# Kernel tuning notes

Measured on AMD Instinct MI355X. Metric: run time of the kernel, lower is better.

The kernel has to match this reference:

```python
import jax, jax.numpy as jnp
import numpy as np
from jax import lax

N, D, K = 8192, 512, 16
EPS = 1e-8


def _safe_sqrt(x):
    # sqrt with a guard so vjp is finite at exact zeros (diagonal of dist matrix)
    return jnp.where(x > 0, jnp.sqrt(jnp.maximum(x, 1e-12)), 0.0)


def _pairwise_dist(a):
    # [n, d] -> [n, n] euclidean distances via Gram trick
    sq = jnp.sum(a * a, axis=-1)
    d2 = sq[:, None] + sq[None, :] - 2.0 * (a @ a.T)
    return _safe_sqrt(d2)


def _curvature_proxy(emb, k):
    n = emb.shape[0]
    dists = _pairwise_dist(emb)  # [n, n]
    neg_d, knn_idx = lax.top_k(-dists, k + 1)  # k+1 smallest
    knn_dists = -neg_d[:, 1:]   # drop self [n, k]
    knn_idx = knn_idx[:, 1:]    # [n, k]
    avg_dist_to_neighbors = knn_dists.mean(axis=1)  # [n]

    nb = emb[knn_idx]  # [n, k, d] gathered neighbor embeddings
    nsq = jnp.sum(nb * nb, axis=-1)  # [n, k]
    gram = jnp.einsum('nkd,nld->nkl', nb, nb)  # [n, k, k]
    inter = _safe_sqrt(nsq[:, :, None] + nsq[:, None, :] - 2.0 * gram)

    mask = jnp.triu(jnp.ones((k, k), dtype=bool), 1)
    n_pairs = k * (k - 1) // 2
    inter_mean = jnp.sum(jnp.where(mask, inter, 0.0), axis=(1, 2)) / n_pairs  # [n]

    curvature = inter_mean / (avg_dist_to_neighbors + EPS)
    return curvature, knn_dists


def setup_inputs() -> dict:
    key = jax.random.key(0)
    k1, k2, k3 = jax.random.split(key, 3)
    embeddings = jax.random.normal(k1, (N, D), dtype=jnp.float32)
    ref_curvature = jax.random.uniform(k2, (N,), dtype=jnp.float32)
    ref_distances = jax.random.uniform(k3, (N, K), dtype=jnp.float32)
    return {"embeddings": embeddings, "ref_curvature": ref_curvature,
            "ref_distances": ref_distances}


def reference(embeddings, ref_curvature, ref_distances):
    curr_curv, curr_dists = _curvature_proxy(embeddings, K)
    curvature_loss = jnp.mean((curr_curv - ref_curvature) ** 2)
    scale_loss = (curr_dists.mean() - ref_distances.mean()) ** 2
    return curvature_loss + 0.1 * scale_loss
```

## Files before the change

kernel.cpp:

```cpp
#include <hip/hip_runtime.h>
#include <cfloat>
#include <cmath>
#include <stdint.h>

#define N 8192
#define D 512
#define K 16
#define RB 64
#define JS 2048
#define NSL (N / JS)
#define JT 128
#define NT (JS / JT)
#define KC 64
#define NCH (D / KC)
#define CAP 32
#define PB 64

typedef __bf16 bf16x8 __attribute__((ext_vector_type(8)));
typedef __bf16 bf16x4 __attribute__((ext_vector_type(4)));
typedef float  f32x16 __attribute__((ext_vector_type(16)));
typedef float  f32x4  __attribute__((ext_vector_type(4)));

__global__ __launch_bounds__(256)
void k_cast_sqnorm(const float* __restrict__ emb, float* __restrict__ sq,
                   __bf16* __restrict__ embh, int* __restrict__ kadjG) {
    int row = blockIdx.x * 4 + (threadIdx.x >> 6);
    int lane = threadIdx.x & 63;
    const float4* e = (const float4*)(emb + (size_t)row * D);
    float s = 0.f;
    #pragma unroll
    for (int c = 0; c < 2; c++) {
        float4 v = e[lane + 64 * c];
        s += v.x * v.x + v.y * v.y + v.z * v.z + v.w * v.w;
        bf16x4 h = { (__bf16)v.x, (__bf16)v.y, (__bf16)v.z, (__bf16)v.w };
        *(bf16x4*)&embh[(size_t)row * D + (size_t)(lane + 64 * c) * 4] = h;
    }
    for (int off = 32; off; off >>= 1) s += __shfl_down(s, off, 64);
    if (lane == 0) sq[row] = s;
    if (lane == 1) kadjG[row] = 0x7f7fffff;
}

__global__ __launch_bounds__(512)
void k_knn(const __bf16* __restrict__ embh, const float* __restrict__ sq,
           float* __restrict__ pd2, int* __restrict__ pidx,
           int* __restrict__ kadjG) {
    __shared__ __align__(16) __bf16 As[2][RB][KC + 8];
    __shared__ __align__(16) __bf16 Bs[2][JT][KC + 8];
    __shared__ float svD[RB][CAP + 1];
    __shared__ int   svI[RB][CAP + 1];
    __shared__ float sqr[RB];
    __shared__ float kadj[RB];
    __shared__ int   scount[RB];
    __shared__ int   again2[2];

    const int t   = threadIdx.x;
    const int rg  = blockIdx.x >> 2;
    const int sl  = blockIdx.x & 3;
    const int ib  = rg * RB;
    const int jsb = sl * JS;
    const int lane = t & 63, quad = lane >> 5, l31 = lane & 31;
    const int w  = t >> 6;
    const int wr = (w & 1) * 32;
    const int wc = (w >> 1) * 32;

    const int mrow = t >> 3, tid8 = t & 7;
    float l0 = FLT_MAX, l1 = FLT_MAX;
    int   i0 = 0, i1 = 0;
    float kmx = FLT_MAX;
    int   nfill = 0;

    if (t < RB) {
        sqr[t] = sq[ib + t];
        kadj[t] = FLT_MAX; scount[t] = 0;
    }
    __syncthreads();

    for (int jt = 0; jt < NT; jt++) {
        const int jb = jsb + jt * JT;
        f32x16 acc = {};

        {
            int row = t >> 3, g = t & 7;
            *(uint4*)&As[0][row][g * 8] = *(const uint4*)&embh[(size_t)(ib + row) * D + g * 8];
            #pragma unroll
            for (int q = 0; q < 2; q++) {
                int s = t + 512 * q;
                int brow = s >> 3, bg = s & 7;
                *(uint4*)&Bs[0][brow][bg * 8] = *(const uint4*)&embh[(size_t)(jb + brow) * D + bg * 8];
            }
        }
        __syncthreads();

        uint4 pfA, pfB[2];
        for (int kc = 0; kc < NCH; kc++) {
            const int cur = kc & 1;
            if (kc + 1 < NCH) {
                int k0 = (kc + 1) * KC;
                {
                    int row = t >> 3, g = t & 7;
                    pfA = *(const uint4*)&embh[(size_t)(ib + row) * D + k0 + g * 8];
                }
                #pragma unroll
                for (int q = 0; q < 2; q++) {
                    int s = t + 512 * q; int brow = s >> 3, bg = s & 7;
                    pfB[q] = *(const uint4*)&embh[(size_t)(jb + brow) * D + k0 + bg * 8];
                }
            }
            __builtin_amdgcn_s_setprio(1);
            #pragma unroll
            for (int kk = 0; kk < KC / 16; kk++) {
                int ko = kk * 16 + quad * 8;
                bf16x8 a0 = *(const bf16x8*)&As[cur][wr + l31][ko];
                bf16x8 b0 = *(const bf16x8*)&Bs[cur][wc + l31][ko];
                acc = __builtin_amdgcn_mfma_f32_32x32x16_bf16(a0, b0, acc, 0, 0, 0);
            }
            __builtin_amdgcn_s_setprio(0);
            if (kc + 1 < NCH) {
                {
                    int row = t >> 3, g = t & 7;
                    *(uint4*)&As[cur ^ 1][row][g * 8] = pfA;
                }
                #pragma unroll
                for (int q = 0; q < 2; q++) {
                    int s = t + 512 * q; int brow = s >> 3, bg = s & 7;
                    *(uint4*)&Bs[cur ^ 1][brow][bg * 8] = pfB[q];
                }
            }
            __syncthreads();
        }

        if (t < RB) {
            float g = __int_as_float(kadjG[ib + t]);
            kadj[t] = fminf(kadj[t], g - sqr[t]);
        }
        if (t == 0) again2[0] = 0;
        __syncthreads();

        float sqc0 = sq[jb + wc + l31];
        uint32_t mask = 0;
        int pass = 0;
        while (true) {
            #pragma unroll
            for (int reg = 0; reg < 16; reg++) {
                if ((mask >> reg) & 1) continue;
                int row_l = wr + ((reg & 3) + ((reg >> 2) << 3) + (quad << 2));
                float t2 = sqc0 - 2.f * acc[reg];
                if (t2 < kadj[row_l]) {
                    int j = jb + wc + l31;
                    if (j != ib + row_l) {
                        int p = atomicAdd(&scount[row_l], 1);
                        if (p < CAP) {
                            svD[row_l][p] = t2 + sqr[row_l];
                            svI[row_l][p] = j;
                            mask |= (1u << reg);
                        }
                    }
                }
            }
            __syncthreads();
            {
                int cnt = scount[mrow];
                if (cnt) {
                    int m = cnt < CAP ? cnt : CAP;
                    for (int p = 0; p < m; p++) {
                        float d2 = svD[mrow][p];
                        if (d2 < kmx) {
                            if (nfill < K) {
                                if ((nfill >> 1) == tid8) {
                                    int jv = svI[mrow][p];
                                    if ((nfill & 1) == 0) { l0 = d2; i0 = jv; }
                                    else                  { l1 = d2; i1 = jv; }
                                }
                                nfill++;
                                if (nfill == K) {
                                    float lm = fmaxf(l0, l1);
                                    #pragma unroll
                                    for (int off = 1; off < 8; off <<= 1)
                                        lm = fmaxf(lm, __shfl_xor(lm, off, 64));
                                    kmx = lm;
                                }
                            } else {
                                float mx = l0; int am = 0;
                                if (l1 > mx) { mx = l1; am = 1; }
                                int gam = (tid8 << 1) | am;
                                #pragma unroll
                                for (int off = 1; off < 8; off <<= 1) {
                                    float omx = __shfl_xor(mx, off, 64);
                                    int   oga = __shfl_xor(gam, off, 64);
                                    if (omx > mx || (omx == mx && oga < gam)) { mx = omx; gam = oga; }
                                }
                                if ((gam >> 1) == tid8) {
                                    int jv = svI[mrow][p];
                                    if ((gam & 1) == 0) { l0 = d2; i0 = jv; }
                                    else                { l1 = d2; i1 = jv; }
                                }
                                float lm = fmaxf(l0, l1);
                                #pragma unroll
                                for (int off = 1; off < 8; off <<= 1)
                                    lm = fmaxf(lm, __shfl_xor(lm, off, 64));
                                kmx = lm;
                            }
                        }
                    }
                    if (tid8 == 0) {
                        kadj[mrow] = fminf(kadj[mrow], kmx - sqr[mrow]);
                        scount[mrow] = 0;
                        if (cnt > CAP) again2[pass & 1] = 1;
                    }
                }
            }
            if (t == 0) again2[(pass + 1) & 1] = 0;
            __syncthreads();
            if (!again2[pass & 1]) break;
            pass++;
        }

        if (tid8 == 0 && kmx < FLT_MAX)
            atomicMin(&kadjG[ib + mrow], __float_as_int(kmx));
    }

    {
        size_t base = (size_t)(ib + mrow) * (NSL * K) + sl * K + tid8 * 2;
        pd2[base + 0] = l0; pd2[base + 1] = l1;
        pidx[base + 0] = i0; pidx[base + 1] = i1;
    }
}

__global__ __launch_bounds__(256)
void k_merge(const float* __restrict__ pd2, const int* __restrict__ pidx,
             int* __restrict__ knn, float* __restrict__ row_sum) {
    int row = blockIdx.x * 256 + threadIdx.x;
    float bd[K]; int bi[K];
    #pragma unroll
    for (int q = 0; q < K; q++) { bd[q] = FLT_MAX; bi[q] = 0; }
    float kmx = FLT_MAX;
    const float* pr = pd2 + (size_t)row * (NSL * K);
    const int*   pi = pidx + (size_t)row * (NSL * K);
    for (int s = 0; s < NSL * K; s++) {
        float d2 = pr[s];
        if (d2 < kmx) {
            int am = 0; float mx = bd[0];
            #pragma unroll
            for (int q = 1; q < K; q++) if (bd[q] > mx) { mx = bd[q]; am = q; }
            bd[am] = d2; bi[am] = pi[s];
            mx = bd[0];
            #pragma unroll
            for (int q = 1; q < K; q++) mx = fmaxf(mx, bd[q]);
            kmx = mx;
        }
    }
    float s = 0.f;
    #pragma unroll
    for (int q = 0; q < K; q++) {
        float d2 = bd[q];
        s += (d2 > 0.f) ? sqrtf(fmaxf(d2, 1e-12f)) : 0.f;
        knn[(size_t)row * K + q] = bi[q];
    }
    row_sum[row] = s;
}

__global__ __launch_bounds__(256)
void k_curv(const __bf16* __restrict__ embh, const int* __restrict__ knn_idx,
            const float* __restrict__ row_sum, const float* __restrict__ ref_curv,
            float* __restrict__ curv_err) {
    __shared__ __align__(16) __bf16 nb[4][K][D + 8];
    __shared__ float diagS[4][16];
    const int t = threadIdx.x;
    const int w = t >> 6, lane = t & 63;
    const int i = blockIdx.x * 4 + w;

    #pragma unroll
    for (int r = 0; r < K; r++) {
        int nidx = knn_idx[(size_t)i * K + r];
        *(uint4*)&nb[w][r][lane * 8] =
            *(const uint4*)&embh[(size_t)nidx * D + lane * 8];
    }
    __syncthreads();

    f32x4 acc = {};
    #pragma unroll
    for (int kc = 0; kc < D / 32; kc++) {
        bf16x8 a = *(const bf16x8*)&nb[w][lane & 15][(lane >> 4) * 8 + kc * 32];
        acc = __builtin_amdgcn_mfma_f32_16x16x32_bf16(a, a, acc, 0, 0, 0);
    }

    #pragma unroll
    for (int q = 0; q < 4; q++) {
        int r = (lane >> 4) * 4 + q;
        if (r == (lane & 15)) diagS[w][r] = acc[q];
    }
    __syncthreads();

    float s = 0.f;
    #pragma unroll
    for (int q = 0; q < 4; q++) {
        int r = (lane >> 4) * 4 + q, c = lane & 15;
        if (r != c) {
            float d2 = diagS[w][r] + diagS[w][c] - 2.f * acc[q];
            s += (d2 > 0.f) ? sqrtf(fmaxf(d2, 1e-12f)) : 0.f;
        }
    }
    #pragma unroll
    for (int off = 32; off; off >>= 1) s += __shfl_down(s, off, 64);

    if (lane == 0) {
        float inter_mean = (0.5f * s) / 120.f;
        float avg = row_sum[i] / 16.f;
        float curv = inter_mean / (avg + 1e-8f);
        float diff = curv - ref_curv[i];
        curv_err[i] = diff * diff;
    }
}

__global__ __launch_bounds__(256)
void k_part(const float* __restrict__ curv_err, const float* __restrict__ row_sum,
            const float* __restrict__ ref_dist, float* __restrict__ part) {
    const int b = blockIdx.x, t = threadIdx.x;
    const int gid = b * 256 + t;
    const int stride = PB * 256;
    float s1 = 0.f, s2 = 0.f, s3 = 0.f;
    for (int i = gid; i < N; i += stride) { s1 += curv_err[i]; s2 += row_sum[i]; }
    for (int i = gid; i < N * K; i += stride) s3 += ref_dist[i];
    for (int off = 32; off; off >>= 1) {
        s1 += __shfl_down(s1, off, 64);
        s2 += __shfl_down(s2, off, 64);
        s3 += __shfl_down(s3, off, 64);
    }
    __shared__ float a1[4], a2[4], a3[4];
    int w = t >> 6, lane = t & 63;
    if (lane == 0) { a1[w] = s1; a2[w] = s2; a3[w] = s3; }
    __syncthreads();
    if (t == 0) {
        float t1 = 0.f, t2 = 0.f, t3 = 0.f;
        #pragma unroll
        for (int q = 0; q < 4; q++) { t1 += a1[q]; t2 += a2[q]; t3 += a3[q]; }
        part[b] = t1; part[PB + b] = t2; part[2 * PB + b] = t3;
    }
}

__global__ __launch_bounds__(64)
void k_final2(const float* __restrict__ part, float* __restrict__ out) {
    const int t = threadIdx.x;
    float s1 = part[t], s2 = part[PB + t], s3 = part[2 * PB + t];
    for (int off = 32; off; off >>= 1) {
        s1 += __shfl_down(s1, off, 64);
        s2 += __shfl_down(s2, off, 64);
        s3 += __shfl_down(s3, off, 64);
    }
    if (t == 0) {
        float curv_loss = s1 / (float)N;
        float dm = s2 / (float)(N * K);
        float rm = s3 / (float)(N * K);
        float d = dm - rm;
        out[0] = curv_loss + 0.1f * d * d;
    }
}

extern "C" void kernel_launch(void* const* d_in, const int* in_sizes, int n_in,
                              void* d_out, int out_size, void* d_ws, size_t ws_size,
                              hipStream_t stream) {
    const float* emb      = (const float*)d_in[0];
    const float* ref_curv = (const float*)d_in[1];
    const float* ref_dist = (const float*)d_in[2];
    float* out = (float*)d_out;

    float*  sq       = (float*)d_ws;
    float*  row_sum  = sq + N;
    float*  curv_err = row_sum + N;
    float*  pd2      = curv_err + N;
    int*    pidx     = (int*)(pd2 + (size_t)N * NSL * K);
    int*    knn      = pidx + (size_t)N * NSL * K;
    __bf16* embh     = (__bf16*)(knn + (size_t)N * K);
    float*  part     = (float*)(embh + (size_t)N * D);
    int*    kadjG    = (int*)(part + 3 * PB);

    k_cast_sqnorm<<<N / 4, 256, 0, stream>>>(emb, sq, embh, kadjG);
    k_knn<<<(N / RB) * NSL, 512, 0, stream>>>(embh, sq, pd2, pidx, kadjG);
    k_merge<<<N / 256, 256, 0, stream>>>(pd2, pidx, knn, row_sum);
    k_curv<<<N / 4, 256, 0, stream>>>(embh, knn, row_sum, ref_curv, curv_err);
    k_part<<<PB, 256, 0, stream>>>(curv_err, row_sum, ref_dist, part);
    k_final2<<<1, 64, 0, stream>>>(part, out);
}
```

Measured before the change: 362.8 us.

## Flatten tile and K-chunk loops into one continuous double-buffered pipeline

Merges the per-column-tile loop and the K-chunk loop into one flattened loop unrolled by two, so the next tile's first chunks are prefetched while the current tile finishes. This removes the pipeline drain and refill at every tile boundary. Barriers now use a custom macro that waits only on LDS counters (lgkmcnt) instead of a full __syncthreads, and the kadjG global read is issued early into a register. The cost is more live prefetch registers and more complex control flow, and the hand-written barrier could miss a needed wait.

```diff
diff --git a/kernel.cpp b/kernel.cpp
--- a/kernel.cpp
+++ b/kernel.cpp
@@ -13,6 +13,7 @@
 #define NT (JS / JT)
 #define KC 64
 #define NCH (D / KC)
+#define TOT (NT * NCH)
 #define CAP 32
 #define PB 64
 
@@ -20,6 +21,12 @@
 typedef __bf16 bf16x4 __attribute__((ext_vector_type(4)));
 typedef float  f32x16 __attribute__((ext_vector_type(16)));
 typedef float  f32x4  __attribute__((ext_vector_type(4)));
+
+#define SYNCK() do {                                          \
+    asm volatile("s_waitcnt lgkmcnt(0)" ::: "memory");        \
+    __builtin_amdgcn_s_barrier();                             \
+    asm volatile("" ::: "memory");                            \
+} while (0)
 
 __global__ __launch_bounds__(256)
 void k_cast_sqnorm(const float* __restrict__ emb, float* __restrict__ sq,
@@ -63,160 +70,194 @@
     const int wr = (w & 1) * 32;
     const int wc = (w >> 1) * 32;
 
+    const int arow = t >> 3, ag = t & 7;
+
     const int mrow = t >> 3, tid8 = t & 7;
     float l0 = FLT_MAX, l1 = FLT_MAX;
     int   i0 = 0, i1 = 0;
     float kmx = FLT_MAX;
     int   nfill = 0;
+    float kg = FLT_MAX;
 
     if (t < RB) {
         sqr[t] = sq[ib + t];
         kadj[t] = FLT_MAX; scount[t] = 0;
     }
-    __syncthreads();
-
-    for (int jt = 0; jt < NT; jt++) {
-        const int jb = jsb + jt * JT;
-        f32x16 acc = {};
-
+
+    f32x16 acc = {};
+    uint4 pfA_e, pfB_e[2];
+    uint4 pfA_o, pfB_o[2];
+
+    {
+        *(uint4*)&As[0][arow][ag * 8] = *(const uint4*)&embh[(size_t)(ib + arow) * D + ag * 8];
+        #pragma unroll
+        for (int q = 0; q < 2; q++) {
+            int s = t + 512 * q; int brow = s >> 3, bg = s & 7;
+            *(uint4*)&Bs[0][brow][bg * 8] = *(const uint4*)&embh[(size_t)(jsb + brow) * D + bg * 8];
+        }
+        pfA_o = *(const uint4*)&embh[(size_t)(ib + arow) * D + KC + ag * 8];
+        #pragma unroll
+        for (int q = 0; q < 2; q++) {
+            int s = t + 512 * q; int brow = s >> 3, bg = s & 7;
+            pfB_o[q] = *(const uint4*)&embh[(size_t)(jsb + brow) * D + KC + bg * 8];
+        }
+    }
+    SYNCK();
+
+    #pragma unroll 1
+    for (int f = 0; f < TOT; f += 2) {
+        if (f + 2 < TOT) {
+            const int g2 = f + 2;
+            const int jb2 = jsb + (g2 >> 3) * JT;
+            const int k02 = (g2 & 7) * KC;
+            pfA_e = *(const uint4*)&embh[(size_t)(ib + arow) * D + k02 + ag * 8];
+            #pragma unroll
+            for (int q = 0; q < 2; q++) {
+                int s = t + 512 * q; int brow = s >> 3, bg = s & 7;
+                pfB_e[q] = *(const uint4*)&embh[(size_t)(jb2 + brow) * D + k02 + bg * 8];
+            }
+        }
+        if ((f & 7) == 0 && t < RB)
+            kg = __int_as_float(kadjG[ib + t]);
+        __builtin_amdgcn_s_setprio(1);
+        #pragma unroll
+        for (int kk = 0; kk < KC / 16; kk++) {
+            int ko = kk * 16 + quad * 8;
+            bf16x8 a0 = *(const bf16x8*)&As[0][wr + l31][ko];
+            bf16x8 b0 = *(const bf16x8*)&Bs[0][wc + l31][ko];
+            acc = __builtin_amdgcn_mfma_f32_32x32x16_bf16(a0, b0, acc, 0, 0, 0);
+        }
+        __builtin_amdgcn_s_setprio(0);
         {
-            int row = t >> 3, g = t & 7;
-            *(uint4*)&As[0][row][g * 8] = *(const uint4*)&embh[(size_t)(ib + row) * D + g * 8];
+            *(uint4*)&As[1][arow][ag * 8] = pfA_o;
             #pragma unroll
             for (int q = 0; q < 2; q++) {
-                int s = t + 512 * q;
-                int brow = s >> 3, bg = s & 7;
-                *(uint4*)&Bs[0][brow][bg * 8] = *(const uint4*)&embh[(size_t)(jb + brow) * D + bg * 8];
+                int s = t + 512 * q; int brow = s >> 3, bg = s & 7;
+                *(uint4*)&Bs[1][brow][bg * 8] = pfB_o[q];
             }
         }
-        __syncthreads();
-
-        uint4 pfA, pfB[2];
-        for (int kc = 0; kc < NCH; kc++) {
-            const int cur = kc & 1;
-            if (kc + 1 < NCH) {
-                int k0 = (kc + 1) * KC;
-                {
-                    int row = t >> 3, g = t & 7;
-                    pfA = *(const uint4*)&embh[(size_t)(ib + row) * D + k0 + g * 8];
-                }
+        SYNCK();
+
+        if (f + 3 < TOT) {
+            const int g2 = f + 3;
+            const int jb2 = jsb + (g2 >> 3) * JT;
+            const int k02 = (g2 & 7) * KC;
+            pfA_o = *(const uint4*)&embh[(size_t)(ib + arow) * D + k02 + ag * 8];
+            #pragma unroll
+            for (int q = 0; q < 2; q++) {
+                int s = t + 512 * q; int brow = s >> 3, bg = s & 7;
+                pfB_o[q] = *(const uint4*)&embh[(size_t)(jb2 + brow) * D + k02 + bg * 8];
+            }
+        }
+        __builtin_amdgcn_s_setprio(1);
+        #pragma unroll
+        for (int kk = 0; kk < KC / 16; kk++) {
+            int ko = kk * 16 + quad * 8;
+            bf16x8 a0 = *(const bf16x8*)&As[1][wr + l31][ko];
+            bf16x8 b0 = *(const bf16x8*)&Bs[1][wc + l31][ko];
+            acc = __builtin_amdgcn_mfma_f32_32x32x16_bf16(a0, b0, acc, 0, 0, 0);
+        }
+        __builtin_amdgcn_s_setprio(0);
+        if (f + 2 < TOT) {
+            *(uint4*)&As[0][arow][ag * 8] = pfA_e;
+            #pragma unroll
+            for (int q = 0; q < 2; q++) {
+                int s = t + 512 * q; int brow = s >> 3, bg = s & 7;
+                *(uint4*)&Bs[0][brow][bg * 8] = pfB_e[q];
+            }
+        }
+        if (((f + 1) & 7) == 7) {
+            if (t < RB) kadj[t] = fminf(kadj[t], kg - sqr[t]);
+            if (t == 0) again2[0] = 0;
+        }
+        SYNCK();
+
+        if (((f + 1) & 7) == 7) {
+            const int jb = jsb + ((f + 1) >> 3) * JT;
+            float sqc0 = sq[jb + wc + l31];
+            uint32_t mask = 0;
+            int pass = 0;
+            while (true) {
                 #pragma unroll
-                for (int q = 0; q < 2; q++) {
-                    int s = t + 512 * q; int brow = s >> 3, bg = s & 7;
-                    pfB[q] = *(const uint4*)&embh[(size_t)(jb + brow) * D + k0 + bg * 8];
-                }
-            }
-            __builtin_amdgcn_s_setprio(1);
-            #pragma unroll
-            for (int kk = 0; kk < KC / 16; kk++) {
-                int ko = kk * 16 + quad * 8;
-                bf16x8 a0 = *(const bf16x8*)&As[cur][wr + l31][ko];
-                bf16x8 b0 = *(const bf16x8*)&Bs[cur][wc + l31][ko];
-                acc = __builtin_amdgcn_mfma_f32_32x32x16_bf16(a0, b0, acc, 0, 0, 0);
-            }
-            __builtin_amdgcn_s_setprio(0);
-            if (kc + 1 < NCH) {
-                {
-                    int row = t >> 3, g = t & 7;
-                    *(uint4*)&As[cur ^ 1][row][g * 8] = pfA;
-                }
-                #pragma unroll
-                for (int q = 0; q < 2; q++) {
-                    int s = t + 512 * q; int brow = s >> 3, bg = s & 7;
-                    *(uint4*)&Bs[cur ^ 1][brow][bg * 8] = pfB[q];
-                }
-            }
-            __syncthreads();
-        }
-
-        if (t < RB) {
-            float g = __int_as_float(kadjG[ib + t]);
-            kadj[t] = fminf(kadj[t], g - sqr[t]);
-        }
-        if (t == 0) again2[0] = 0;
-        __syncthreads();
-
-        float sqc0 = sq[jb + wc + l31];
-        uint32_t mask = 0;
-        int pass = 0;
-        while (true) {
-            #pragma unroll
-            for (int reg = 0; reg < 16; reg++) {
-                if ((mask >> reg) & 1) continue;
-                int row_l = wr + ((reg & 3) + ((reg >> 2) << 3) + (quad << 2));
-                float t2 = sqc0 - 2.f * acc[reg];
-                if (t2 < kadj[row_l]) {
-                    int j = jb + wc + l31;
-                    if (j != ib + row_l) {
-                        int p = atomicAdd(&scount[row_l], 1);
-                        if (p < CAP) {
-                            svD[row_l][p] = t2 + sqr[row_l];
-                            svI[row_l][p] = j;
-                            mask |= (1u << reg);
+                for (int reg = 0; reg < 16; reg++) {
+                    if ((mask >> reg) & 1) continue;
+                    int row_l = wr + ((reg & 3) + ((reg >> 2) << 3) + (quad << 2));
+                    float t2 = sqc0 - 2.f * acc[reg];
+                    if (t2 < kadj[row_l]) {
+                        int j = jb + wc + l31;
+                        if (j != ib + row_l) {
+                            int p = atomicAdd(&scount[row_l], 1);
+                            if (p < CAP) {
+                                svD[row_l][p] = t2 + sqr[row_l];
+                                svI[row_l][p] = j;
+                                mask |= (1u << reg);
+                            }
                         }
                     }
                 }
-            }
-            __syncthreads();
-            {
-                int cnt = scount[mrow];
-                if (cnt) {
-                    int m = cnt < CAP ? cnt : CAP;
-                    for (int p = 0; p < m; p++) {
-                        float d2 = svD[mrow][p];
-                        if (d2 < kmx) {
-                            if (nfill < K) {
-                                if ((nfill >> 1) == tid8) {
-                                    int jv = svI[mrow][p];
-                                    if ((nfill & 1) == 0) { l0 = d2; i0 = jv; }
-                                    else                  { l1 = d2; i1 = jv; }
-                                }
-                                nfill++;
-                                if (nfill == K) {
+                __syncthreads();
+                {
+                    int cnt = scount[mrow];
+                    if (cnt) {
+                        int m = cnt < CAP ? cnt : CAP;
+                        for (int p = 0; p < m; p++) {
+                            float d2 = svD[mrow][p];
+                            if (d2 < kmx) {
+                                if (nfill < K) {
+                                    if ((nfill >> 1) == tid8) {
+                                        int jv = svI[mrow][p];
+                                        if ((nfill & 1) == 0) { l0 = d2; i0 = jv; }
+                                        else                  { l1 = d2; i1 = jv; }
+                                    }
+                                    nfill++;
+                                    if (nfill == K) {
+                                        float lm = fmaxf(l0, l1);
+                                        #pragma unroll
+                                        for (int off = 1; off < 8; off <<= 1)
+                                            lm = fmaxf(lm, __shfl_xor(lm, off, 64));
+                                        kmx = lm;
+                                    }
+                                } else {
+                                    float mx = l0; int am = 0;
+                                    if (l1 > mx) { mx = l1; am = 1; }
+                                    int gam = (tid8 << 1) | am;
+                                    #pragma unroll
+                                    for (int off = 1; off < 8; off <<= 1) {
+                                        float omx = __shfl_xor(mx, off, 64);
+                                        int   oga = __shfl_xor(gam, off, 64);
+                                        if (omx > mx || (omx == mx && oga < gam)) { mx = omx; gam = oga; }
+                                    }
+                                    if ((gam >> 1) == tid8) {
+                                        int jv = svI[mrow][p];
+                                        if ((gam & 1) == 0) { l0 = d2; i0 = jv; }
+                                        else                { l1 = d2; i1 = jv; }
+                                    }
                                     float lm = fmaxf(l0, l1);
                                     #pragma unroll
                                     for (int off = 1; off < 8; off <<= 1)
                                         lm = fmaxf(lm, __shfl_xor(lm, off, 64));
                                     kmx = lm;
                                 }
-                            } else {
-                                float mx = l0; int am = 0;
-                                if (l1 > mx) { mx = l1; am = 1; }
-                                int gam = (tid8 << 1) | am;
-                                #pragma unroll
-                                for (int off = 1; off < 8; off <<= 1) {
-                                    float omx = __shfl_xor(mx, off, 64);
-                                    int   oga = __shfl_xor(gam, off, 64);
-                                    if (omx > mx || (omx == mx && oga < gam)) { mx = omx; gam = oga; }
-                                }
-                                if ((gam >> 1) == tid8) {
-                                    int jv = svI[mrow][p];
-                                    if ((gam & 1) == 0) { l0 = d2; i0 = jv; }
-                                    else                { l1 = d2; i1 = jv; }
-                                }
-                                float lm = fmaxf(l0, l1);
-                                #pragma unroll
-                                for (int off = 1; off < 8; off <<= 1)
-                                    lm = fmaxf(lm, __shfl_xor(lm, off, 64));
-                                kmx = lm;
                             }
                         }
-                    }
-                    if (tid8 == 0) {
-                        kadj[mrow] = fminf(kadj[mrow], kmx - sqr[mrow]);
-                        scount[mrow] = 0;
-                        if (cnt > CAP) again2[pass & 1] = 1;
+                        if (tid8 == 0) {
+                            kadj[mrow] = fminf(kadj[mrow], kmx - sqr[mrow]);
+                            scount[mrow] = 0;
+                            if (cnt > CAP) again2[pass & 1] = 1;
+                        }
                     }
                 }
+                if (t == 0) again2[(pass + 1) & 1] = 0;
+                __syncthreads();
+                if (!again2[pass & 1]) break;
+                pass++;
             }
-            if (t == 0) again2[(pass + 1) & 1] = 0;
-            __syncthreads();
-            if (!again2[pass & 1]) break;
-            pass++;
-        }
-
-        if (tid8 == 0 && kmx < FLT_MAX)
-            atomicMin(&kadjG[ib + mrow], __float_as_int(kmx));
+
+            if (tid8 == 0 && kmx < FLT_MAX)
+                atomicMin(&kadjG[ib + mrow], __float_as_int(kmx));
+
+            acc = (f32x16){};
+        }
     }
 
     {
```

Measured after the change: 542.9 us. 49.7% more time.
